# Performance work log

Measured on AMD Instinct MI355X. Metric: run time of the kernel, lower is better.

## Reference

```python
import jax, jax.numpy as jnp
import numpy as np

N, FR, P, B = 8192, 128, 4194304, 64
LH1, LH2 = 128, 64

def _mlp(x, W1, b1, W2, b2, W3, b3):
    h = jnp.tanh(x @ W1 + b1)
    h = jnp.tanh(h @ W2 + b2)
    return h @ W3 + b3  # [N, 1]

def setup_inputs() -> dict:
    key = jax.random.key(0)
    ks = jax.random.split(key, 12)
    r = jax.random.normal(ks[0], (N, FR), jnp.float32)
    xyz = jax.random.uniform(ks[1], (N, 3), jnp.float32) * 60.0  # box so distances >> sigma
    p0 = jax.random.randint(ks[2], (P,), 0, N)
    off = jax.random.randint(ks[3], (P,), 1, N)  # avoid self-pairs (D2=0)
    pairs = jnp.stack([p0, (p0 + off) % N], axis=1).astype(jnp.int32)
    num_pairs = jnp.full((B,), P // B, dtype=jnp.int32)
    def lin(k, fin, fout):
        return (jax.random.normal(k, (fin, fout), jnp.float32) / np.sqrt(fin)).astype(jnp.float32)
    sW1, sW2, sW3 = lin(ks[4], FR, LH1), lin(ks[5], LH1, LH2), lin(ks[6], LH2, 1)
    eW1, eW2, eW3 = lin(ks[7], FR, LH1), lin(ks[8], LH1, LH2), lin(ks[9], LH2, 1)
    z1, z2, z3 = jnp.zeros((LH1,), jnp.float32), jnp.zeros((LH2,), jnp.float32), jnp.zeros((1,), jnp.float32)
    return dict(r=r, xyz=xyz, pairs=pairs, num_pairs=num_pairs,
                sW1=sW1, sb1=z1, sW2=sW2, sb2=z2, sW3=sW3, sb3=z3,
                eW1=eW1, eb1=z1, eW2=eW2, eb2=z2, eW3=eW3, eb3=z3)

def reference(r, xyz, pairs, num_pairs, sW1, sb1, sW2, sb2, sW3, sb3,
              eW1, eb1, eW2, eb2, eW3, eb3):
    # D2 gathered at pairs == squared distance between the two atoms of each pair
    dx = xyz[pairs[:, 1]] - xyz[pairs[:, 0]]          # [P, 3]
    D2 = jnp.sum(dx * dx, axis=1, keepdims=True)       # [P, 1]
    inv_D = D2 ** -0.5
    sigma = 4.0 + 10.0 * _mlp(r, sW1, sb1, sW2, sb2, sW3, sb3) ** 2   # [N, 1]
    epsilon = 0.1 * _mlp(r, eW1, eb1, eW2, eb2, eW3, eb3) ** 2        # [N, 1]
    sigma_mixed = jnp.sqrt(sigma[pairs[:, 0]] * sigma[pairs[:, 1]])    # [P, 1]
    epsilon_mixed = jnp.sqrt(epsilon[pairs[:, 0]] * epsilon[pairs[:, 1]])
    s = sigma_mixed * inv_D
    s6 = s ** 6
    E_pair = 4.0 * epsilon_mixed * (s6 * s6 - s6)       # [P, 1]
    seg = jnp.repeat(jnp.arange(B), num_pairs, total_repeat_length=P)
    E = jax.ops.segment_sum(E_pair, seg, num_segments=B)  # [B, 1]
    return E
```

## Files before the change

### kernel.cpp

```cpp
#include <hip/hip_runtime.h>
#include <hip/hip_fp16.h>

#define NATOM 8192
#define FR    128
#define NSEG  64
#define PB    256
#define PT    1024
#define PPT   16

typedef _Float16 v8h __attribute__((ext_vector_type(8)));
typedef _Float16 v4h __attribute__((ext_vector_type(4)));
typedef float    v4f __attribute__((ext_vector_type(4)));

__device__ __forceinline__ float fast_tanh(float x)
{
    float t = __expf(2.f * x);
    return 1.f - 2.f * __builtin_amdgcn_rcpf(t + 1.f);
}

__global__ __launch_bounds__(512) void k_prep(
    const float* __restrict__ w1s, const float* __restrict__ w1e,
    const float* __restrict__ w2s, const float* __restrict__ w2e,
    _Float16* __restrict__ planes)
{
    int i = blockIdx.x * 512 + threadIdx.x;
    if (i < 32768) {
        int c = i >> 7, k = i & 127;
        float x = (c < 128) ? w1s[k * 128 + c] : w1e[k * 128 + (c - 128)];
        _Float16 h = (_Float16)x;
        planes[i] = h;
        planes[32768 + i] = (_Float16)((x - (float)h) * 4096.f);
    } else if (i < 49152) {
        int u = i - 32768;
        int c = u >> 7, k = u & 127;
        float x = (c < 64) ? w2s[k * 64 + c] : w2e[k * 64 + (c - 64)];
        _Float16 h = (_Float16)x;
        planes[65536 + u] = h;
        planes[81920 + u] = (_Float16)((x - (float)h) * 4096.f);
    }
}

__global__ __launch_bounds__(512) void k_mm(
    const float* __restrict__ r, const float* __restrict__ xyz,
    const _Float16* __restrict__ planes,
    const float* __restrict__ b1s, const float* __restrict__ b1e,
    const float* __restrict__ b2s, const float* __restrict__ b2e,
    const float* __restrict__ w3s, const float* __restrict__ w3e,
    const float* __restrict__ b3s, const float* __restrict__ b3e,
    float4* __restrict__ atomd)
{
    extern __shared__ char ldsraw[];
    _Float16* Wh  = (_Float16*)ldsraw;
    _Float16* Wl  = Wh + 32768;
    _Float16* h1h = Wh;
    _Float16* h1l = Wh + 16384;
    _Float16* W2h = Wh + 32768;
    _Float16* W2l = Wh + 49152;
    float*    mArr = (float*)(ldsraw + 131072);

    const int tid = threadIdx.x;
    const int a0  = blockIdx.x * 64;
    const int l = tid & 63, wv = tid >> 6;
    const int row16 = l & 15, kgrp = l >> 4;
    const int at = wv & 3, chf = wv >> 2;

    {
        const uint4* ph = (const uint4*)planes;
        const uint4* pl = (const uint4*)(planes + 32768);
        uint4* dh = (uint4*)Wh; uint4* dl = (uint4*)Wl;
#pragma unroll
        for (int i = 0; i < 8; ++i) {
            int g = i * 512 + tid;
            int c = g >> 4, ch = g & 15;
            int sw = c * 16 + (ch ^ (c & 15));
            dh[sw] = ph[g]; dl[sw] = pl[g];
        }
    }

    v8h rh[4], rl[4];
    {
        const float* rb = r + (size_t)(a0 + at * 16 + row16) * FR + kgrp * 8;
#pragma unroll
        for (int ks = 0; ks < 4; ++ks) {
            float4 x0 = *(const float4*)(rb + ks * 32);
            float4 x1 = *(const float4*)(rb + ks * 32 + 4);
            float xs[8] = {x0.x, x0.y, x0.z, x0.w, x1.x, x1.y, x1.z, x1.w};
#pragma unroll
            for (int j = 0; j < 8; ++j) {
                _Float16 h = (_Float16)xs[j];
                rh[ks][j] = h;
                rl[ks][j] = (_Float16)((xs[j] - (float)h) * 4096.f);
            }
        }
    }
    __syncthreads();

    v4h hpack[8], lpack[8];
    {
#pragma unroll
        for (int ct = 0; ct < 8; ++ct) {
            int crow = chf * 128 + ct * 16 + row16;
            v4f a = {0.f, 0.f, 0.f, 0.f}, cr = {0.f, 0.f, 0.f, 0.f};
            int rbo = crow * 128, sw = crow & 15;
#pragma unroll
            for (int ks = 0; ks < 4; ++ks) {
                int off = rbo + (((ks * 4 + kgrp) ^ sw) * 8);
                v8h wh = *(const v8h*)(Wh + off);
                v8h wl = *(const v8h*)(Wl + off);
                a  = __builtin_amdgcn_mfma_f32_16x16x32_f16(wh, rh[ks], a,  0, 0, 0);
                cr = __builtin_amdgcn_mfma_f32_16x16x32_f16(wh, rl[ks], cr, 0, 0, 0);
                cr = __builtin_amdgcn_mfma_f32_16x16x32_f16(wl, rh[ks], cr, 0, 0, 0);
            }
            int colb = chf * 128 + ct * 16 + kgrp * 4;
            const float* bp = (colb < 128) ? (b1s + colb) : (b1e + (colb - 128));
            float4 bv = *(const float4*)bp;
            float bvx[4] = {bv.x, bv.y, bv.z, bv.w};
#pragma unroll
            for (int j = 0; j < 4; ++j) {
                float v = fast_tanh(a[j] + cr[j] * 2.44140625e-4f + bvx[j]);
                _Float16 h = (_Float16)v;
                hpack[ct][j] = h;
                lpack[ct][j] = (_Float16)((v - (float)h) * 4096.f);
            }
        }
    }
    __syncthreads();

    {
        int arow = at * 16 + row16;
#pragma unroll
        for (int ct = 0; ct < 8; ++ct) {
            int colb = chf * 128 + ct * 16 + kgrp * 4;
            int chs = (colb >> 3) ^ row16;
            int off = arow * 256 + chs * 8 + (colb & 7);
            *(v4h*)(h1h + off) = hpack[ct];
            *(v4h*)(h1l + off) = lpack[ct];
        }
        const uint4* ph = (const uint4*)(planes + 65536);
        const uint4* pl = (const uint4*)(planes + 81920);
        uint4* dh = (uint4*)W2h; uint4* dl = (uint4*)W2l;
#pragma unroll
        for (int i = 0; i < 4; ++i) {
            int g = i * 512 + tid;
            int c = g >> 4, ch = g & 15;
            int sw = c * 16 + (ch ^ (c & 15));
            dh[sw] = ph[g]; dl[sw] = pl[g];
        }
    }
    __syncthreads();

    {
        const int arow = at * 16 + row16;
        v8h bh[4], bl[4];
#pragma unroll
        for (int ks = 0; ks < 4; ++ks) {
            int chunk = chf * 16 + ks * 4 + kgrp;
            int off = arow * 256 + ((chunk ^ row16) * 8);
            bh[ks] = *(const v8h*)(h1h + off);
            bl[ks] = *(const v8h*)(h1l + off);
        }
        float ps = 0.f;
#pragma unroll
        for (int ct2 = 0; ct2 < 4; ++ct2) {
            int c2 = chf * 64 + ct2 * 16 + row16;
            v4f a = {0.f, 0.f, 0.f, 0.f}, cr = {0.f, 0.f, 0.f, 0.f};
            int rbo = c2 * 128, sw = c2 & 15;
#pragma unroll
            for (int ks = 0; ks < 4; ++ks) {
                int off = rbo + (((ks * 4 + kgrp) ^ sw) * 8);
                v8h wh = *(const v8h*)(W2h + off);
                v8h wl = *(const v8h*)(W2l + off);
                a  = __builtin_amdgcn_mfma_f32_16x16x32_f16(wh, bh[ks], a,  0, 0, 0);
                cr = __builtin_amdgcn_mfma_f32_16x16x32_f16(wh, bl[ks], cr, 0, 0, 0);
                cr = __builtin_amdgcn_mfma_f32_16x16x32_f16(wl, bh[ks], cr, 0, 0, 0);
            }
            int cb = ct2 * 16 + kgrp * 4;
            float4 b2v = *(const float4*)((chf ? b2e : b2s) + cb);
            float4 w3v = *(const float4*)((chf ? w3e : w3s) + cb);
            float b2x[4] = {b2v.x, b2v.y, b2v.z, b2v.w};
            float w3x[4] = {w3v.x, w3v.y, w3v.z, w3v.w};
#pragma unroll
            for (int j = 0; j < 4; ++j) {
                float h2 = fast_tanh(a[j] + cr[j] * 2.44140625e-4f + b2x[j]);
                ps = fmaf(h2, w3x[j], ps);
            }
        }
        ps += __shfl_xor(ps, 16);
        ps += __shfl_xor(ps, 32);
        if (l < 16) mArr[chf * 64 + at * 16 + l] = ps + (chf ? b3e[0] : b3s[0]);
    }
    __syncthreads();

    if (tid < 64) {
        int atom = a0 + tid;
        float ms = mArr[tid], me = mArr[64 + tid];
        float sg = fmaf(10.f * ms, ms, 4.f);
        float p  = sg * sqrtf(sg);
        float q  = 0.31622776601683794f * fabsf(me);
        __half2 pq = __halves2half2(__float2half(p), __float2half(q));
        atomd[atom] = make_float4(xyz[3 * atom], xyz[3 * atom + 1],
                                  xyz[3 * atom + 2], __builtin_bit_cast(float, pq));
    }
}

__device__ __forceinline__ float pair_e(const float4* atomd, int ia, int ib)
{
    float4 A = atomd[ia], B = atomd[ib];
    float dx = A.x - B.x, dy = A.y - B.y, dz = A.z - B.z;
    float D2 = fmaf(dx, dx, fmaf(dy, dy, dz * dz));
    float inv = __builtin_amdgcn_rcpf(D2);
    float inv3 = inv * inv * inv;
    __half2 ha = __builtin_bit_cast(__half2, A.w);
    __half2 hb = __builtin_bit_cast(__half2, B.w);
    float pp = __low2float(ha) * __low2float(hb);
    float qq = __high2float(ha) * __high2float(hb);
    float s6 = pp * pp * inv3;
    return 4.f * qq * (s6 * s6 - s6);
}

__global__ __launch_bounds__(PT, 1) void k_pair(
    const float4* __restrict__ atomg, const int* __restrict__ pairs,
    const int* __restrict__ num_pairs,
    float* __restrict__ blocksums, int P)
{
    extern __shared__ char smem[];
    float4* atomd = (float4*)smem;
    int*    off   = (int*)(smem + NATOM * 16);
    float*  bsum  = (float*)(smem + NATOM * 16 + 68 * 4);

    const int tid = threadIdx.x;

#pragma unroll
    for (int i = 0; i < NATOM / PT; ++i) atomd[i * PT + tid] = atomg[i * PT + tid];
    if (tid < 64) {
        int run = num_pairs[tid];
#pragma unroll
        for (int d = 1; d < 64; d <<= 1) {
            int o = __shfl_up(run, d);
            if (tid >= d) run += o;
        }
        off[tid + 1] = run;
        if (tid == 0) off[0] = 0;
        bsum[tid] = 0.f;
    }
    __syncthreads();

    const int base = (blockIdx.x * PT + tid) * PPT;
    const bool fast = (base + PPT <= P);

    if (__all(fast)) {
        int pr2[PPT * 2];
        const int4* pp4 = (const int4*)(pairs + (size_t)base * 2);
#pragma unroll
        for (int i = 0; i < PPT / 2; ++i) {
            int4 v = pp4[i];
            pr2[4*i] = v.x; pr2[4*i+1] = v.y; pr2[4*i+2] = v.z; pr2[4*i+3] = v.w;
        }
        int s = 0;
#pragma unroll
        for (int st = 32; st; st >>= 1) { int ns = s + st; if (ns <= NSEG - 1 && off[ns] <= base) s = ns; }
        float acc = 0.f;
        if (base + PPT <= off[s + 1] || s == NSEG - 1) {
#pragma unroll
            for (int i = 0; i < PPT; ++i)
                acc += pair_e(atomd, pr2[2 * i], pr2[2 * i + 1]);
        } else {
            int off_next = off[s + 1];
#pragma unroll
            for (int i = 0; i < PPT; ++i) {
                int idx = base + i;
                while (s < NSEG - 1 && idx >= off_next) {
                    if (acc != 0.f) atomicAdd(&bsum[s], acc);
                    acc = 0.f; ++s; off_next = off[s + 1];
                }
                acc += pair_e(atomd, pr2[2 * i], pr2[2 * i + 1]);
            }
        }
        int s0 = __builtin_amdgcn_readfirstlane(s);
        if (__all(s == s0)) {
            float v = acc;
#pragma unroll
            for (int o = 32; o; o >>= 1) v += __shfl_xor(v, o);
            if ((tid & 63) == 0) atomicAdd(&bsum[s0], v);
        } else {
            atomicAdd(&bsum[s], acc);
        }
    } else if (base < P) {
        int s = 0;
#pragma unroll
        for (int st = 32; st; st >>= 1) { int ns = s + st; if (ns <= NSEG - 1 && off[ns] <= base) s = ns; }
        int off_next = off[s + 1];
        float acc = 0.f;
        for (int i = 0; i < PPT; ++i) {
            int idx = base + i;
            if (idx >= P) break;
            while (s < NSEG - 1 && idx >= off_next) {
                if (acc != 0.f) atomicAdd(&bsum[s], acc);
                acc = 0.f; ++s; off_next = off[s + 1];
            }
            acc += pair_e(atomd, pairs[2 * (size_t)idx], pairs[2 * (size_t)idx + 1]);
        }
        if (acc != 0.f) atomicAdd(&bsum[s], acc);
    }
    __syncthreads();
    if (tid < NSEG) blocksums[blockIdx.x * NSEG + tid] = bsum[tid];
}

__global__ __launch_bounds__(512) void k_reduce(const float* __restrict__ bs, float* __restrict__ out)
{
    __shared__ float red[8][NSEG];
    int b = threadIdx.x & 63, part = threadIdx.x >> 6;
    float s = 0.f;
    for (int j = part; j < PB; j += 8) s += bs[(size_t)j * NSEG + b];
    red[part][b] = s;
    __syncthreads();
    if (threadIdx.x < NSEG) {
        float t = 0.f;
#pragma unroll
        for (int p = 0; p < 8; ++p) t += red[p][threadIdx.x];
        out[threadIdx.x] = t;
    }
}

extern "C" void kernel_launch(void* const* d_in, const int* in_sizes, int n_in,
                              void* d_out, int out_size, void* d_ws, size_t ws_size,
                              hipStream_t stream)
{
    const float* r    = (const float*)d_in[0];
    const float* xyz  = (const float*)d_in[1];
    const int*   prs  = (const int*)d_in[2];
    const int*   np   = (const int*)d_in[3];
    const float* sW1  = (const float*)d_in[4];
    const float* sb1  = (const float*)d_in[5];
    const float* sW2  = (const float*)d_in[6];
    const float* sb2  = (const float*)d_in[7];
    const float* sW3  = (const float*)d_in[8];
    const float* sb3  = (const float*)d_in[9];
    const float* eW1  = (const float*)d_in[10];
    const float* eb1  = (const float*)d_in[11];
    const float* eW2  = (const float*)d_in[12];
    const float* eb2  = (const float*)d_in[13];
    const float* eW3  = (const float*)d_in[14];
    const float* eb3  = (const float*)d_in[15];
    float* out = (float*)d_out;
    const int P = in_sizes[2] / 2;

    _Float16* planes = (_Float16*)d_ws;
    float4*   atomd  = (float4*)((char*)d_ws + 196608);
    float*    bsums  = (float*)((char*)d_ws + 196608 + 131072);

    k_prep<<<96, 512, 0, stream>>>(sW1, eW1, sW2, eW2, planes);

    size_t smem1 = 131072 + 512;
    hipFuncSetAttribute((const void*)k_mm, hipFuncAttributeMaxDynamicSharedMemorySize, (int)smem1);
    k_mm<<<NATOM / 64, 512, smem1, stream>>>(r, xyz, planes, sb1, eb1, sb2, eb2,
                                             sW3, eW3, sb3, eb3, atomd);

    size_t smem = (size_t)NATOM * 16 + 68 * 4 + NSEG * 4;
    hipFuncSetAttribute((const void*)k_pair, hipFuncAttributeMaxDynamicSharedMemorySize, (int)smem);
    k_pair<<<PB, PT, smem, stream>>>(atomd, prs, np, bsums, P);
    k_reduce<<<1, 512, 0, stream>>>(bsums, out);
}
```

Baseline: 37.92 us.

## Halve atoms per MLP block and prefetch pair indices before LDS staging

The MLP kernel now handles 32 atoms per block instead of 64, doubling the grid to fill more CUs. Output columns are split into quarters across waves, and the layer-3 partial sums are combined in a final step. Each block still stages the full weight planes into LDS, so total weight traffic doubles. Separately, the pair kernel issues its global loads of pair indices before the LDS atom-table fill and barrier, so that memory latency overlaps with the staging.

```diff
diff --git a/kernel.cpp b/kernel.cpp
--- a/kernel.cpp
+++ b/kernel.cpp
@@ -53,16 +53,16 @@
     _Float16* Wh  = (_Float16*)ldsraw;
     _Float16* Wl  = Wh + 32768;
     _Float16* h1h = Wh;
-    _Float16* h1l = Wh + 16384;
-    _Float16* W2h = Wh + 32768;
-    _Float16* W2l = Wh + 49152;
+    _Float16* h1l = Wh + 8192;
+    _Float16* W2h = Wh + 16384;
+    _Float16* W2l = Wh + 32768;
     float*    mArr = (float*)(ldsraw + 131072);
 
     const int tid = threadIdx.x;
-    const int a0  = blockIdx.x * 64;
+    const int a0  = blockIdx.x * 32;
     const int l = tid & 63, wv = tid >> 6;
     const int row16 = l & 15, kgrp = l >> 4;
-    const int at = wv & 3, chf = wv >> 2;
+    const int at = wv & 1, cq = wv >> 1;
 
     {
         const uint4* ph = (const uint4*)planes;
@@ -95,11 +95,11 @@
     }
     __syncthreads();
 
-    v4h hpack[8], lpack[8];
-    {
-#pragma unroll
-        for (int ct = 0; ct < 8; ++ct) {
-            int crow = chf * 128 + ct * 16 + row16;
+    v4h hpack[4], lpack[4];
+    {
+#pragma unroll
+        for (int ct = 0; ct < 4; ++ct) {
+            int crow = cq * 64 + ct * 16 + row16;
             v4f a = {0.f, 0.f, 0.f, 0.f}, cr = {0.f, 0.f, 0.f, 0.f};
             int rbo = crow * 128, sw = crow & 15;
 #pragma unroll
@@ -111,7 +111,7 @@
                 cr = __builtin_amdgcn_mfma_f32_16x16x32_f16(wh, rl[ks], cr, 0, 0, 0);
                 cr = __builtin_amdgcn_mfma_f32_16x16x32_f16(wl, rh[ks], cr, 0, 0, 0);
             }
-            int colb = chf * 128 + ct * 16 + kgrp * 4;
+            int colb = cq * 64 + ct * 16 + kgrp * 4;
             const float* bp = (colb < 128) ? (b1s + colb) : (b1e + (colb - 128));
             float4 bv = *(const float4*)bp;
             float bvx[4] = {bv.x, bv.y, bv.z, bv.w};
@@ -129,8 +129,8 @@
     {
         int arow = at * 16 + row16;
 #pragma unroll
-        for (int ct = 0; ct < 8; ++ct) {
-            int colb = chf * 128 + ct * 16 + kgrp * 4;
+        for (int ct = 0; ct < 4; ++ct) {
+            int colb = cq * 64 + ct * 16 + kgrp * 4;
             int chs = (colb >> 3) ^ row16;
             int off = arow * 256 + chs * 8 + (colb & 7);
             *(v4h*)(h1h + off) = hpack[ct];
@@ -150,19 +150,20 @@
     __syncthreads();
 
     {
+        const int path = cq >> 1, half = cq & 1;
         const int arow = at * 16 + row16;
         v8h bh[4], bl[4];
 #pragma unroll
         for (int ks = 0; ks < 4; ++ks) {
-            int chunk = chf * 16 + ks * 4 + kgrp;
+            int chunk = path * 16 + ks * 4 + kgrp;
             int off = arow * 256 + ((chunk ^ row16) * 8);
             bh[ks] = *(const v8h*)(h1h + off);
             bl[ks] = *(const v8h*)(h1l + off);
         }
         float ps = 0.f;
 #pragma unroll
-        for (int ct2 = 0; ct2 < 4; ++ct2) {
-            int c2 = chf * 64 + ct2 * 16 + row16;
+        for (int ct2 = 0; ct2 < 2; ++ct2) {
+            int c2 = path * 64 + half * 32 + ct2 * 16 + row16;
             v4f a = {0.f, 0.f, 0.f, 0.f}, cr = {0.f, 0.f, 0.f, 0.f};
             int rbo = c2 * 128, sw = c2 & 15;
 #pragma unroll
@@ -174,9 +175,9 @@
                 cr = __builtin_amdgcn_mfma_f32_16x16x32_f16(wh, bl[ks], cr, 0, 0, 0);
                 cr = __builtin_amdgcn_mfma_f32_16x16x32_f16(wl, bh[ks], cr, 0, 0, 0);
             }
-            int cb = ct2 * 16 + kgrp * 4;
-            float4 b2v = *(const float4*)((chf ? b2e : b2s) + cb);
-            float4 w3v = *(const float4*)((chf ? w3e : w3s) + cb);
+            int cb = half * 32 + ct2 * 16 + kgrp * 4;
+            float4 b2v = *(const float4*)((path ? b2e : b2s) + cb);
+            float4 w3v = *(const float4*)((path ? w3e : w3s) + cb);
             float b2x[4] = {b2v.x, b2v.y, b2v.z, b2v.w};
             float w3x[4] = {w3v.x, w3v.y, w3v.z, w3v.w};
 #pragma unroll
@@ -187,13 +188,14 @@
         }
         ps += __shfl_xor(ps, 16);
         ps += __shfl_xor(ps, 32);
-        if (l < 16) mArr[chf * 64 + at * 16 + l] = ps + (chf ? b3e[0] : b3s[0]);
-    }
-    __syncthreads();
-
-    if (tid < 64) {
+        if (l < 16) mArr[cq * 32 + at * 16 + l] = ps;
+    }
+    __syncthreads();
+
+    if (tid < 32) {
         int atom = a0 + tid;
-        float ms = mArr[tid], me = mArr[64 + tid];
+        float ms = mArr[tid] + mArr[32 + tid] + b3s[0];
+        float me = mArr[64 + tid] + mArr[96 + tid] + b3e[0];
         float sg = fmaf(10.f * ms, ms, 4.f);
         float p  = sg * sqrtf(sg);
         float q  = 0.31622776601683794f * fabsf(me);
@@ -229,6 +231,18 @@
     float*  bsum  = (float*)(smem + NATOM * 16 + 68 * 4);
 
     const int tid = threadIdx.x;
+    const int base = (blockIdx.x * PT + tid) * PPT;
+    const bool fastall = __all(base + PPT <= P);
+
+    int pr2[PPT * 2];
+    if (fastall) {
+        const int4* pp4 = (const int4*)(pairs + (size_t)base * 2);
+#pragma unroll
+        for (int i = 0; i < PPT / 2; ++i) {
+            int4 v = pp4[i];
+            pr2[4*i] = v.x; pr2[4*i+1] = v.y; pr2[4*i+2] = v.z; pr2[4*i+3] = v.w;
+        }
+    }
 
 #pragma unroll
     for (int i = 0; i < NATOM / PT; ++i) atomd[i * PT + tid] = atomg[i * PT + tid];
@@ -245,17 +259,7 @@
     }
     __syncthreads();
 
-    const int base = (blockIdx.x * PT + tid) * PPT;
-    const bool fast = (base + PPT <= P);
-
-    if (__all(fast)) {
-        int pr2[PPT * 2];
-        const int4* pp4 = (const int4*)(pairs + (size_t)base * 2);
-#pragma unroll
-        for (int i = 0; i < PPT / 2; ++i) {
-            int4 v = pp4[i];
-            pr2[4*i] = v.x; pr2[4*i+1] = v.y; pr2[4*i+2] = v.z; pr2[4*i+3] = v.w;
-        }
+    if (fastall) {
         int s = 0;
 #pragma unroll
         for (int st = 32; st; st >>= 1) { int ns = s + st; if (ns <= NSEG - 1 && off[ns] <= base) s = ns; }
@@ -353,7 +357,7 @@
 
     size_t smem1 = 131072 + 512;
     hipFuncSetAttribute((const void*)k_mm, hipFuncAttributeMaxDynamicSharedMemorySize, (int)smem1);
-    k_mm<<<NATOM / 64, 512, smem1, stream>>>(r, xyz, planes, sb1, eb1, sb2, eb2,
+    k_mm<<<NATOM / 32, 512, smem1, stream>>>(r, xyz, planes, sb1, eb1, sb2, eb2,
                                              sW3, eW3, sb3, eb3, atomd);
 
     size_t smem = (size_t)NATOM * 16 + 68 * 4 + NSEG * 4;
```

Measured after the change: 38.86 us. 1.02x slower.

## Fuse weight split into MLP kernel and replace reduce kernel with atomics

Applied to the files above, without the earlier changes.

Drops the separate weight-prep kernel: each MLP block now reads the fp32 weights directly, splits them into fp16 hi/lo planes and writes them swizzled into LDS. Drops the final reduce kernel: each pair block atomically adds its per-segment sums into the output, which is zeroed first with a memset. This removes two launches and the workspace round trip. In exchange every MLP block redoes the weight conversion with strided global loads, and the result now depends on atomic ordering.

```diff
diff --git a/kernel.cpp b/kernel.cpp
--- a/kernel.cpp
+++ b/kernel.cpp
@@ -18,35 +18,14 @@
     return 1.f - 2.f * __builtin_amdgcn_rcpf(t + 1.f);
 }
 
-__global__ __launch_bounds__(512) void k_prep(
-    const float* __restrict__ w1s, const float* __restrict__ w1e,
-    const float* __restrict__ w2s, const float* __restrict__ w2e,
-    _Float16* __restrict__ planes)
-{
-    int i = blockIdx.x * 512 + threadIdx.x;
-    if (i < 32768) {
-        int c = i >> 7, k = i & 127;
-        float x = (c < 128) ? w1s[k * 128 + c] : w1e[k * 128 + (c - 128)];
-        _Float16 h = (_Float16)x;
-        planes[i] = h;
-        planes[32768 + i] = (_Float16)((x - (float)h) * 4096.f);
-    } else if (i < 49152) {
-        int u = i - 32768;
-        int c = u >> 7, k = u & 127;
-        float x = (c < 64) ? w2s[k * 64 + c] : w2e[k * 64 + (c - 64)];
-        _Float16 h = (_Float16)x;
-        planes[65536 + u] = h;
-        planes[81920 + u] = (_Float16)((x - (float)h) * 4096.f);
-    }
-}
-
 __global__ __launch_bounds__(512) void k_mm(
     const float* __restrict__ r, const float* __restrict__ xyz,
-    const _Float16* __restrict__ planes,
-    const float* __restrict__ b1s, const float* __restrict__ b1e,
-    const float* __restrict__ b2s, const float* __restrict__ b2e,
-    const float* __restrict__ w3s, const float* __restrict__ w3e,
-    const float* __restrict__ b3s, const float* __restrict__ b3e,
+    const float* __restrict__ w1s, const float* __restrict__ b1s,
+    const float* __restrict__ w2s, const float* __restrict__ b2s,
+    const float* __restrict__ w3s, const float* __restrict__ b3s,
+    const float* __restrict__ w1e, const float* __restrict__ b1e,
+    const float* __restrict__ w2e, const float* __restrict__ b2e,
+    const float* __restrict__ w3e, const float* __restrict__ b3e,
     float4* __restrict__ atomd)
 {
     extern __shared__ char ldsraw[];
@@ -64,17 +43,22 @@
     const int row16 = l & 15, kgrp = l >> 4;
     const int at = wv & 3, chf = wv >> 2;
 
-    {
-        const uint4* ph = (const uint4*)planes;
-        const uint4* pl = (const uint4*)(planes + 32768);
-        uint4* dh = (uint4*)Wh; uint4* dl = (uint4*)Wl;
-#pragma unroll
-        for (int i = 0; i < 8; ++i) {
-            int g = i * 512 + tid;
-            int c = g >> 4, ch = g & 15;
-            int sw = c * 16 + (ch ^ (c & 15));
-            dh[sw] = ph[g]; dl[sw] = pl[g];
-        }
+#pragma unroll
+    for (int i = 0; i < 8; ++i) {
+        int g = i * 512 + tid;
+        int c = g & 255, ch = g >> 8;
+        const float* wp = (c < 128) ? (w1s + c) : (w1e + (c - 128));
+        v8h hh, ll;
+#pragma unroll
+        for (int j = 0; j < 8; ++j) {
+            float x = wp[(ch * 8 + j) * 128];
+            _Float16 h = (_Float16)x;
+            hh[j] = h;
+            ll[j] = (_Float16)((x - (float)h) * 4096.f);
+        }
+        int sw = c * 16 + (ch ^ (c & 15));
+        *(v8h*)(Wh + sw * 8) = hh;
+        *(v8h*)(Wl + sw * 8) = ll;
     }
 
     v8h rh[4], rl[4];
@@ -96,32 +80,30 @@
     __syncthreads();
 
     v4h hpack[8], lpack[8];
-    {
-#pragma unroll
-        for (int ct = 0; ct < 8; ++ct) {
-            int crow = chf * 128 + ct * 16 + row16;
-            v4f a = {0.f, 0.f, 0.f, 0.f}, cr = {0.f, 0.f, 0.f, 0.f};
-            int rbo = crow * 128, sw = crow & 15;
-#pragma unroll
-            for (int ks = 0; ks < 4; ++ks) {
-                int off = rbo + (((ks * 4 + kgrp) ^ sw) * 8);
-                v8h wh = *(const v8h*)(Wh + off);
-                v8h wl = *(const v8h*)(Wl + off);
-                a  = __builtin_amdgcn_mfma_f32_16x16x32_f16(wh, rh[ks], a,  0, 0, 0);
-                cr = __builtin_amdgcn_mfma_f32_16x16x32_f16(wh, rl[ks], cr, 0, 0, 0);
-                cr = __builtin_amdgcn_mfma_f32_16x16x32_f16(wl, rh[ks], cr, 0, 0, 0);
-            }
-            int colb = chf * 128 + ct * 16 + kgrp * 4;
-            const float* bp = (colb < 128) ? (b1s + colb) : (b1e + (colb - 128));
-            float4 bv = *(const float4*)bp;
-            float bvx[4] = {bv.x, bv.y, bv.z, bv.w};
-#pragma unroll
-            for (int j = 0; j < 4; ++j) {
-                float v = fast_tanh(a[j] + cr[j] * 2.44140625e-4f + bvx[j]);
-                _Float16 h = (_Float16)v;
-                hpack[ct][j] = h;
-                lpack[ct][j] = (_Float16)((v - (float)h) * 4096.f);
-            }
+#pragma unroll
+    for (int ct = 0; ct < 8; ++ct) {
+        int crow = chf * 128 + ct * 16 + row16;
+        v4f a = {0.f, 0.f, 0.f, 0.f}, cr = {0.f, 0.f, 0.f, 0.f};
+        int rbo = crow * 128, sw = crow & 15;
+#pragma unroll
+        for (int ks = 0; ks < 4; ++ks) {
+            int off = rbo + (((ks * 4 + kgrp) ^ sw) * 8);
+            v8h wh = *(const v8h*)(Wh + off);
+            v8h wl = *(const v8h*)(Wl + off);
+            a  = __builtin_amdgcn_mfma_f32_16x16x32_f16(wh, rh[ks], a,  0, 0, 0);
+            cr = __builtin_amdgcn_mfma_f32_16x16x32_f16(wh, rl[ks], cr, 0, 0, 0);
+            cr = __builtin_amdgcn_mfma_f32_16x16x32_f16(wl, rh[ks], cr, 0, 0, 0);
+        }
+        int colb = chf * 128 + ct * 16 + kgrp * 4;
+        const float* bp = (colb < 128) ? (b1s + colb) : (b1e + (colb - 128));
+        float4 bv = *(const float4*)bp;
+        float bvx[4] = {bv.x, bv.y, bv.z, bv.w};
+#pragma unroll
+        for (int j = 0; j < 4; ++j) {
+            float v = fast_tanh(a[j] + cr[j] * 2.44140625e-4f + bvx[j]);
+            _Float16 h = (_Float16)v;
+            hpack[ct][j] = h;
+            lpack[ct][j] = (_Float16)((v - (float)h) * 4096.f);
         }
     }
     __syncthreads();
@@ -136,15 +118,22 @@
             *(v4h*)(h1h + off) = hpack[ct];
             *(v4h*)(h1l + off) = lpack[ct];
         }
-        const uint4* ph = (const uint4*)(planes + 65536);
-        const uint4* pl = (const uint4*)(planes + 81920);
-        uint4* dh = (uint4*)W2h; uint4* dl = (uint4*)W2l;
 #pragma unroll
         for (int i = 0; i < 4; ++i) {
             int g = i * 512 + tid;
-            int c = g >> 4, ch = g & 15;
+            int c = g & 127, ch = g >> 7;
+            const float* wp = (c < 64) ? (w2s + c) : (w2e + (c - 64));
+            v8h hh, ll;
+#pragma unroll
+            for (int j = 0; j < 8; ++j) {
+                float x = wp[(ch * 8 + j) * 64];
+                _Float16 h = (_Float16)x;
+                hh[j] = h;
+                ll[j] = (_Float16)((x - (float)h) * 4096.f);
+            }
             int sw = c * 16 + (ch ^ (c & 15));
-            dh[sw] = ph[g]; dl[sw] = pl[g];
+            *(v8h*)(W2h + sw * 8) = hh;
+            *(v8h*)(W2l + sw * 8) = ll;
         }
     }
     __syncthreads();
@@ -221,7 +210,7 @@
 __global__ __launch_bounds__(PT, 1) void k_pair(
     const float4* __restrict__ atomg, const int* __restrict__ pairs,
     const int* __restrict__ num_pairs,
-    float* __restrict__ blocksums, int P)
+    float* __restrict__ out, int P)
 {
     extern __shared__ char smem[];
     float4* atomd = (float4*)smem;
@@ -303,23 +292,7 @@
         if (acc != 0.f) atomicAdd(&bsum[s], acc);
     }
     __syncthreads();
-    if (tid < NSEG) blocksums[blockIdx.x * NSEG + tid] = bsum[tid];
-}
-
-__global__ __launch_bounds__(512) void k_reduce(const float* __restrict__ bs, float* __restrict__ out)
-{
-    __shared__ float red[8][NSEG];
-    int b = threadIdx.x & 63, part = threadIdx.x >> 6;
-    float s = 0.f;
-    for (int j = part; j < PB; j += 8) s += bs[(size_t)j * NSEG + b];
-    red[part][b] = s;
-    __syncthreads();
-    if (threadIdx.x < NSEG) {
-        float t = 0.f;
-#pragma unroll
-        for (int p = 0; p < 8; ++p) t += red[p][threadIdx.x];
-        out[threadIdx.x] = t;
-    }
+    if (tid < NSEG) atomicAdd(&out[tid], bsum[tid]);
 }
 
 extern "C" void kernel_launch(void* const* d_in, const int* in_sizes, int n_in,
@@ -345,19 +318,16 @@
     float* out = (float*)d_out;
     const int P = in_sizes[2] / 2;
 
-    _Float16* planes = (_Float16*)d_ws;
-    float4*   atomd  = (float4*)((char*)d_ws + 196608);
-    float*    bsums  = (float*)((char*)d_ws + 196608 + 131072);
-
-    k_prep<<<96, 512, 0, stream>>>(sW1, eW1, sW2, eW2, planes);
+    float4* atomd = (float4*)d_ws;
+
+    hipMemsetAsync(out, 0, (size_t)out_size * sizeof(float), stream);
 
     size_t smem1 = 131072 + 512;
     hipFuncSetAttribute((const void*)k_mm, hipFuncAttributeMaxDynamicSharedMemorySize, (int)smem1);
-    k_mm<<<NATOM / 64, 512, smem1, stream>>>(r, xyz, planes, sb1, eb1, sb2, eb2,
-                                             sW3, eW3, sb3, eb3, atomd);
+    k_mm<<<NATOM / 64, 512, smem1, stream>>>(r, xyz, sW1, sb1, sW2, sb2, sW3, sb3,
+                                             eW1, eb1, eW2, eb2, eW3, eb3, atomd);
 
     size_t smem = (size_t)NATOM * 16 + 68 * 4 + NSEG * 4;
     hipFuncSetAttribute((const void*)k_pair, hipFuncAttributeMaxDynamicSharedMemorySize, (int)smem);
-    k_pair<<<PB, PT, smem, stream>>>(atomd, prs, np, bsums, P);
-    k_reduce<<<1, 512, 0, stream>>>(bsums, out);
-}
+    k_pair<<<PB, PT, smem, stream>>>(atomd, prs, np, out, P);
+}
```

Result: faster. 34.79 us (-8.2%).
